# Kernel tuning notes

Hardware: AMD Instinct MI355X
Metric: run time of the kernel (lower is better)

Reference implementation:

```python
import jax, jax.numpy as jnp
import numpy as np

B, FIN, N, K, FOUT = 8, 64, 2048, 20, 128
BN_EPS = 1e-5
LEAKY_SLOPE = 0.01


def _conv2d(x, w, b):
    # x: [B,C,H,W], w: [O,I,kh,kw] -> valid conv, stride 1
    y = jax.lax.conv_general_dilated(
        x, w, window_strides=(1, 1), padding='VALID',
        dimension_numbers=('NCHW', 'OIHW', 'NCHW'))
    return y + b[None, :, None, None]


def _batchnorm(x, gamma, beta):
    # training-mode BN: batch stats over (B,H,W), biased variance (torch default)
    mean = jnp.mean(x, axis=(0, 2, 3), keepdims=True)
    var = jnp.var(x, axis=(0, 2, 3), keepdims=True)
    xn = (x - mean) * jax.lax.rsqrt(var + BN_EPS)
    return xn * gamma[None, :, None, None] + beta[None, :, None, None]


def _edge_features(x, k):
    # x: [B, D, N] -> [B, 2D, N, k]
    xt = jnp.transpose(x, (0, 2, 1))                      # [B,N,D]
    sq = jnp.sum(xt * xt, axis=-1)                        # [B,N]
    dist = sq[:, :, None] + sq[:, None, :] - 2.0 * jnp.einsum('bnd,bmd->bnm', xt, xt)
    # smallest k+1 distances (self is the smallest); drop self
    _, idx = jax.lax.top_k(-dist, k + 1)                  # [B,N,k+1]
    idx = idx[:, :, 1:]                                   # [B,N,k]
    nb = jax.vmap(lambda pts, ind: pts[ind])(xt, idx)     # [B,N,k,D]
    neighbors = jnp.transpose(nb, (0, 3, 1, 2))           # [B,D,N,k]
    central = x[:, :, :, None]                            # [B,D,N,1]
    central_k = jnp.broadcast_to(central, neighbors.shape)
    return jnp.concatenate([central_k, neighbors - central], axis=1)


def setup_inputs() -> dict:
    key = jax.random.key(0)
    ks = jax.random.split(key, 4)
    x = jax.random.normal(ks[0], (B, FIN, N), dtype=jnp.float32)
    conv1_w = jax.random.normal(ks[1], (4 * FIN, 2 * FIN, 1, K // 2 + 1), dtype=jnp.float32) * 0.02
    conv1_b = jnp.zeros((4 * FIN,), jnp.float32)
    bn1_g = jnp.ones((4 * FIN,), jnp.float32)
    bn1_b = jnp.zeros((4 * FIN,), jnp.float32)
    conv2_w = jax.random.normal(ks[2], (2 * FOUT, 2 * FIN, 1, 2 * K), dtype=jnp.float32) * 0.02
    conv2_b = jnp.zeros((2 * FOUT,), jnp.float32)
    bn2_g = jnp.ones((2 * FOUT,), jnp.float32)
    bn2_b = jnp.zeros((2 * FOUT,), jnp.float32)
    return {"x": x, "conv1_w": conv1_w, "conv1_b": conv1_b, "bn1_g": bn1_g,
            "bn1_b": bn1_b, "conv2_w": conv2_w, "conv2_b": conv2_b,
            "bn2_g": bn2_g, "bn2_b": bn2_b, "k": K}


def reference(x, conv1_w, conv1_b, bn1_g, bn1_b, conv2_w, conv2_b, bn2_g, bn2_b, k):
    ee = _edge_features(x, k)                             # [B,2Fin,N,k]
    Bb, CC, NN, KK = ee.shape
    # inte_conv_hk: conv [1, k//2+1] -> [B,4Fin,N,k/2], BN, LeakyReLU
    h = _batchnorm(_conv2d(ee, conv1_w, conv1_b), bn1_g, bn1_b)
    h = jnp.where(h > 0, h, LEAKY_SLOPE * h)
    # transpose/view dance: [B,N,4Fin,k/2] -> [B,N,2Fin,k] -> [B,2Fin,N,k]
    inte = jnp.transpose(h, (0, 2, 1, 3)).reshape(Bb, NN, CC, KK)
    inte = jnp.transpose(inte, (0, 2, 1, 3))
    merge = jnp.concatenate([ee, inte], axis=3)           # [B,2Fin,N,2k]
    y = _batchnorm(_conv2d(merge, conv2_w, conv2_b), bn2_g, bn2_b)
    y = jax.nn.relu(y)                                    # [B,2Fout,N,1]
    fout = y.shape[1] // 2
    return y.reshape(Bb, fout, 2 * NN)                    # [B,Fout,2N]
```

## Files before the change

kernel.cpp:

```cpp
#include <hip/hip_runtime.h>
#include <stdint.h>

typedef unsigned int uint;
typedef unsigned short ushort;
typedef __attribute__((ext_vector_type(8))) short short8;
typedef __attribute__((ext_vector_type(4))) float f32x4;

__device__ __forceinline__ uint f2bf(float f) {
  uint u = __float_as_uint(f);
  return (u + 0x7fffu + ((u >> 16) & 1u)) >> 16;
}
__device__ __forceinline__ float bf2f(uint us) {
  return __uint_as_float(us << 16);
}
__device__ __forceinline__ int lt_count(unsigned long long m) {
  return (int)__builtin_amdgcn_mbcnt_hi((uint)(m >> 32),
             __builtin_amdgcn_mbcnt_lo((uint)m, 0u));
}

__global__ __launch_bounds__(256) void prep_weights(
    const float* __restrict__ w1, const float* __restrict__ w2,
    ushort* __restrict__ wp1, ushort* __restrict__ wpack) {
  int g = blockIdx.x * 256 + threadIdx.x;
  if (g < 196608) {
    int chunk = g >> 9;
    int r = g & 511;
    int lane = r >> 3, j = r & 7;
    int tks = chunk >> 4;
    int ctile = chunk & 15;
    int t = tks >> 1, ks = tks & 1;
    int c = ctile * 16 + (lane & 15);
    int d = ks * 32 + ((lane >> 4) << 3) + j;
    float val;
    if (t < 11) {
      val = w1[c * 1408 + (64 + d) * 11 + t];
    } else {
      float s = 0.f;
      for (int tt = 0; tt < 11; ++tt)
        s += w1[c * 1408 + d * 11 + tt] - w1[c * 1408 + (64 + d) * 11 + tt];
      val = s;
    }
    wp1[g] = (ushort)f2bf(val);
  } else {
    int gp = g - 196608;
    int chunk = gp >> 9;
    int r = gp & 511;
    int lane = r >> 3, j = r & 7;
    int kb = chunk >> 5;
    int rem = chunk & 31;
    int ks = rem >> 4, ctile = rem & 15;
    int c = ctile * 16 + (lane & 15);
    int k = kb * 64 + ks * 32 + ((lane >> 4) << 3) + j;
    float val;
    if (k < 64) {
      int d = k;
      float s = 0.f;
      for (int jn = 0; jn < 20; ++jn)
        s += w2[c * 5120 + d * 40 + jn] - w2[c * 5120 + (64 + d) * 40 + jn];
      val = s;
    } else if (k < 1344) {
      int q = k - 64; int jn = q >> 6, d = q & 63;
      val = w2[c * 5120 + (64 + d) * 40 + jn];
    } else {
      int q = k - 1344; int ci = q / 20, jj = q - ci * 20;
      val = w2[c * 5120 + ci * 40 + 20 + jj];
    }
    wpack[gp] = (ushort)f2bf(val);
  }
}

__global__ __launch_bounds__(256) void transpose_x(const float* __restrict__ x,
                                                   uint* __restrict__ xtu,
                                                   float* __restrict__ xtf,
                                                   float* __restrict__ sqf) {
  __shared__ float t[64][65];
  int tid = threadIdx.x;
  int blk = blockIdx.x;
  int b = blk >> 5, n0 = (blk & 31) << 6;
  const float* xb = x + b * 131072;
  #pragma unroll
  for (int it = 0; it < 16; ++it) {
    int d = (it << 2) + (tid >> 6);
    int n = tid & 63;
    t[d][n] = xb[d * 2048 + n0 + n];
  }
  __syncthreads();
  #pragma unroll
  for (int it = 0; it < 8; ++it) {
    int n = (it << 3) + (tid >> 5);
    int dp = tid & 31;
    float f0 = t[2 * dp][n], f1 = t[2 * dp + 1][n];
    uint v = f2bf(f0) | (f2bf(f1) << 16);
    size_t col = (size_t)(b * 2048 + n0 + n);
    xtu[col * 32 + dp] = v;
    float2 fv; fv.x = f0; fv.y = f1;
    *(float2*)&xtf[(col << 6) + 2 * dp] = fv;
    float s = f0 * f0 + f1 * f1;
    #pragma unroll
    for (int off = 16; off > 0; off >>= 1) s += __shfl_xor(s, off);
    if (dp == 0) sqf[col] = s;
  }
}

__global__ __launch_bounds__(1024) void knn_kernel(
    const ushort* __restrict__ xbf_t, const float* __restrict__ sqf,
    int* __restrict__ cbuf) {
  __shared__ uint dist[16][1024];
  __shared__ uint surv[16][132];
  int tid = threadIdx.x;
  int wv = tid >> 6, lane = tid & 63;
  int grp = blockIdx.x >> 1;
  int half = blockIdx.x & 1;
  int cbase = half << 10;
  int row0 = grp << 4;
  int b = row0 >> 11, n0 = row0 & 2047;
  const ushort* xt = xbf_t + ((size_t)b << 17);
  const float* sqb = sqf + (b << 11);
  int m = lane & 15, quad = lane >> 4;
  short8 afr0 = *(const short8*)(xt + ((size_t)(n0 + m) << 6) + quad * 8);
  short8 afr1 = *(const short8*)(xt + ((size_t)(n0 + m) << 6) + 32 + quad * 8);
  for (int t = 0; t < 4; ++t) {
    int lcol = (((wv << 2) + t) << 4) + m;
    int col = cbase + lcol;
    short8 bfr0 = *(const short8*)(xt + ((size_t)col << 6) + quad * 8);
    short8 bfr1 = *(const short8*)(xt + ((size_t)col << 6) + 32 + quad * 8);
    f32x4 c = {};
    c = __builtin_amdgcn_mfma_f32_16x16x32_bf16(afr0, bfr0, c, 0, 0, 0);
    c = __builtin_amdgcn_mfma_f32_16x16x32_bf16(afr1, bfr1, c, 0, 0, 0);
    float sq = sqb[col];
    #pragma unroll
    for (int r = 0; r < 4; ++r) {
      float f = sq - 2.f * c[r];
      uint u = __float_as_uint(f);
      uint srt = u ^ ((uint)((int)u >> 31) | 0x80000000u);
      dist[quad * 4 + r][lcol] = (srt & 0xFFFFF800u) | (uint)col;
    }
  }
  __syncthreads();
  uint* dr = dist[wv];
  int selfl = (n0 + wv) - cbase;
  if (selfl >= 0 && selfl < 1024 && ((selfl & 63) == lane))
    dr[selfl] = 0xFFFFFFFFu;

  uint key[16];
  uint v0 = 0xFFFFFFFFu;
  #pragma unroll
  for (int l = 0; l < 16; ++l) {
    uint v = dr[(l << 6) + lane];
    key[l] = v;
    v0 = v0 < v ? v0 : v;
  }

  uint s = v0;
  #pragma unroll
  for (int k = 2; k <= 64; k <<= 1) {
    #pragma unroll
    for (int j = k >> 1; j > 0; j >>= 1) {
      uint o = (uint)__shfl_xor((int)s, j);
      bool up = ((lane & k) == 0);
      bool lower = ((lane & j) == 0);
      uint mn = s < o ? s : o;
      uint mx = s < o ? o : s;
      s = (lower == up) ? mn : mx;
    }
  }
  uint T = (uint)__shfl((int)s, 31);

  int base = 0;
  #pragma unroll
  for (int l = 0; l < 16; ++l) {
    uint v = key[l];
    bool f = (v <= T);
    unsigned long long mk = __ballot(f);
    if (f) {
      int pos = base + lt_count(mk);
      if (pos < 128) surv[wv][pos] = v;
    }
    base += __popcll(mk);
  }
  int S = base < 128 ? base : 128;
  if (lane < 4) surv[wv][S + lane] = 0xFFFFFFFFu;

  int outb = (row0 + wv) * 64 + (half << 5);
  uint k0 = (lane < S) ? surv[wv][lane] : 0xFFFFFFFFu;
  int r0 = 0;
  if (S > 64) {
    uint k1 = (lane + 64 < S) ? surv[wv][lane + 64] : 0xFFFFFFFFu;
    int r1 = 0;
    for (int i = 0; i < S; i += 4) {
      uint4 q = *(const uint4*)&surv[wv][i];
      r0 += (q.x < k0) + (q.y < k0) + (q.z < k0) + (q.w < k0);
      r1 += (q.x < k1) + (q.y < k1) + (q.z < k1) + (q.w < k1);
    }
    if (lane + 64 < S && r1 < 32) cbuf[outb + r1] = (int)(k1 & 2047u);
  } else {
    for (int i = 0; i < S; i += 4) {
      uint4 q = *(const uint4*)&surv[wv][i];
      r0 += (q.x < k0) + (q.y < k0) + (q.z < k0) + (q.w < k0);
    }
  }
  if (lane < S && r0 < 32) cbuf[outb + r0] = (int)(k0 & 2047u);
}

__global__ __launch_bounds__(256) void knn_merge(
    const float* __restrict__ xtf, const int* __restrict__ cbuf,
    int* __restrict__ idxout) {
  __shared__ double dkey[4][64];
  __shared__ int ccol[4][64];
  int tid = threadIdx.x;
  int wv = tid >> 6, lane = tid & 63;
  int row = (blockIdx.x << 2) + wv;
  int b = row >> 11, n = row & 2047;
  int ci = cbuf[row * 64 + lane];
  const float* xc = xtf + ((size_t)b << 17);
  const float4* xj4 = (const float4*)(xc + ((size_t)ci << 6));
  const float4* xi4 = (const float4*)(xc + ((size_t)n << 6));
  double dt = 0.0, s2 = 0.0;
  #pragma unroll 4
  for (int d4 = 0; d4 < 16; ++d4) {
    float4 vj = xj4[d4];
    float4 vi = xi4[d4];
    double a0 = (double)vj.x, a1 = (double)vj.y, a2 = (double)vj.z, a3 = (double)vj.w;
    s2 += a0 * a0 + a1 * a1 + a2 * a2 + a3 * a3;
    dt += (double)vi.x * a0 + (double)vi.y * a1 + (double)vi.z * a2 + (double)vi.w * a3;
  }
  dkey[wv][lane] = s2 - 2.0 * dt;
  ccol[wv][lane] = ci;
  __syncthreads();
  double kl = dkey[wv][lane];
  int rank = 0;
  for (int mm = 0; mm < 64; ++mm) {
    double km = dkey[wv][mm];
    int cm = ccol[wv][mm];
    if (km < kl || (km == kl && cm < ci)) ++rank;
  }
  if (rank < 20) idxout[row * 20 + rank] = ci;
}

__global__ __launch_bounds__(512, 4) void conv1_mfma(
    const ushort* __restrict__ xbf_t, const int* __restrict__ idxbuf,
    const ushort* __restrict__ wp1, uint* __restrict__ hu,
    float* __restrict__ stats) {
  __shared__ ushort sl[21][8][16][8];
  __shared__ int nidx[16][20];
  int tid = threadIdx.x;
  int p0 = blockIdx.x << 4;
  int b = p0 >> 11, n0 = p0 & 2047;
  const ushort* xt = xbf_t + ((size_t)b << 17);
  for (int v = tid; v < 320; v += 512) {
    int p = v / 20, j = v - p * 20;
    nidx[p][j] = idxbuf[(p0 + p) * 20 + j];
  }
  __syncthreads();
  for (int v = tid; v < 2688; v += 512) {
    int s = v >> 7;
    int r = v & 127;
    int p = r >> 3, i = r & 7;
    int col = (s == 0) ? (n0 + p) : nidx[p][s - 1];
    *(short8*)&sl[s][i][p ^ i][0] =
        *(const short8*)(xt + ((size_t)col << 6) + (i << 3));
  }
  __syncthreads();
  int lane = tid & 63, wave = tid >> 6;
  int m = lane & 15, quad = lane >> 4;
  #pragma unroll 1
  for (int pass = 0; pass < 2; ++pass) {
    int ctile = (pass << 3) + wave;
    int c = ctile * 16 + m;
    f32x4 acc[10] = {};
    f32x4 cacc = {};
    #pragma unroll 1
    for (int ks = 0; ks < 2; ++ks) {
      int cch = ks * 4 + quad;
      int ms = m ^ cch;
      short8 tb[11];
      #pragma unroll
      for (int t = 0; t < 11; ++t)
        tb[t] = *(const short8*)(wp1 + (((t * 2 + ks) * 16 + ctile) << 9) + lane * 8);
      short8 ub = *(const short8*)(wp1 + (((22 + ks) * 16 + ctile) << 9) + lane * 8);
      {
        short8 a = *(const short8*)&sl[0][cch][ms][0];
        cacc = __builtin_amdgcn_mfma_f32_16x16x32_bf16(a, ub, cacc, 0, 0, 0);
      }
      #pragma unroll
      for (int s = 1; s <= 20; ++s) {
        short8 a = *(const short8*)&sl[s][cch][ms][0];
        #pragma unroll
        for (int t = 0; t < 11; ++t) {
          int ko = s - 1 - t;
          if (ko >= 0 && ko < 10)
            acc[ko] = __builtin_amdgcn_mfma_f32_16x16x32_bf16(a, tb[t], acc[ko], 0, 0, 0);
        }
      }
    }
    float sacc = 0.f, ssacc = 0.f;
    #pragma unroll
    for (int r = 0; r < 4; ++r) {
      int p = (quad << 2) + r;
      int base5 = ((p0 + p) * 256 + c) * 5;
      float cc = cacc[r];
      #pragma unroll
      for (int q = 0; q < 5; ++q) {
        float f0 = acc[2 * q][r] + cc;
        float f1 = acc[2 * q + 1][r] + cc;
        sacc += f0 + f1;
        ssacc += f0 * f0 + f1 * f1;
        hu[base5 + q] = f2bf(f0) | (f2bf(f1) << 16);
      }
    }
    sacc += __shfl_xor(sacc, 16);  sacc += __shfl_xor(sacc, 32);
    ssacc += __shfl_xor(ssacc, 16); ssacc += __shfl_xor(ssacc, 32);
    if (quad == 0) {
      atomicAdd(&stats[c], sacc);
      atomicAdd(&stats[256 + c], ssacc);
    }
  }
}

__global__ void finalize_kernel(const float* __restrict__ stats,
                                const float* __restrict__ gamma,
                                const float* __restrict__ beta,
                                float* __restrict__ coef, float inv_count) {
  int c = threadIdx.x;
  float m = stats[c] * inv_count;
  float var = stats[256 + c] * inv_count - m * m;
  float a = gamma[c] * rsqrtf(var + 1e-5f);
  coef[c] = a;
  coef[256 + c] = beta[c] - m * a;
}

__global__ __launch_bounds__(512) void conv2_mfma(
    const ushort* __restrict__ xbf_t, const int* __restrict__ idxbuf,
    const uint* __restrict__ hu, const float* __restrict__ coef1,
    const ushort* __restrict__ wpack, float* __restrict__ yraw,
    float* __restrict__ stats) {
  __shared__ ushort As[2][4][64][72];
  __shared__ int nidx[64][20];
  __shared__ float cf[512];
  int tid = threadIdx.x;
  int p0 = blockIdx.x << 6;
  int b = p0 >> 11, n0 = p0 & 2047;
  const ushort* xt = xbf_t + ((size_t)b << 17);

  cf[tid] = coef1[tid];
  for (int v = tid; v < 1280; v += 512) {
    int p = v / 20, j = v - p * 20;
    nidx[p][j] = idxbuf[(p0 + p) * 20 + j];
  }
  __syncthreads();

  int pp = tid >> 3;
  int off = (tid & 7) << 3;

  auto build = [&](int phase, int buf) {
    int kb0 = phase << 2;
    short8 xv[4];
    uint4 hv[4];
    #pragma unroll
    for (int kc = 0; kc < 4; ++kc) {
      int kb = kb0 + kc;
      if (kb >= 61) continue;
      if (kb < 21) {
        int col = (kb == 0) ? (n0 + pp) : nidx[pp][kb - 1];
        xv[kc] = *(const short8*)(xt + ((size_t)col << 6) + off);
      } else {
        int q0 = (kb - 21) * 64 + off;
        hv[kc] = *(const uint4*)(hu + (size_t)(p0 + pp) * 1280 + (q0 >> 1));
      }
    }
    #pragma unroll
    for (int kc = 0; kc < 4; ++kc) {
      int kb = kb0 + kc;
      if (kb >= 61) continue;
      if (kb < 21) {
        *(short8*)&As[buf][kc][pp][off] = xv[kc];
      } else {
        int q0 = (kb - 21) * 64 + off;
        uint4 hvv = hv[kc];
        float f[8];
        f[0] = bf2f(hvv.x & 0xffffu); f[1] = bf2f(hvv.x >> 16);
        f[2] = bf2f(hvv.y & 0xffffu); f[3] = bf2f(hvv.y >> 16);
        f[4] = bf2f(hvv.z & 0xffffu); f[5] = bf2f(hvv.z >> 16);
        f[6] = bf2f(hvv.w & 0xffffu); f[7] = bf2f(hvv.w >> 16);
        ushort o[8];
        #pragma unroll
        for (int i = 0; i < 8; ++i) {
          int ch = (q0 + i) / 10;
          float vv = f[i] * cf[ch] + cf[256 + ch];
          vv = vv > 0.f ? vv : 0.01f * vv;
          o[i] = (ushort)f2bf(vv);
        }
        *(short8*)&As[buf][kc][pp][off] = *(short8*)o;
      }
    }
  };

  int lane = tid & 63, wave = tid >> 6;
  int m = lane & 15, quad = lane >> 4;
  f32x4 acc[4][2] = {};

  build(0, 0);
  __syncthreads();
  for (int phase = 0; phase < 16; ++phase) {
    int buf = phase & 1;
    if (phase < 15) build(phase + 1, buf ^ 1);
    #pragma unroll
    for (int kc = 0; kc < 4; ++kc) {
      int kb = (phase << 2) + kc;
      if (kb >= 61) break;
      #pragma unroll
      for (int ks = 0; ks < 2; ++ks) {
        short8 afr[4];
        #pragma unroll
        for (int mt = 0; mt < 4; ++mt)
          afr[mt] = *(const short8*)&As[buf][kc][mt * 16 + m][ks * 32 + quad * 8];
        #pragma unroll
        for (int nt = 0; nt < 2; ++nt) {
          const ushort* bp = wpack +
              (((size_t)((kb * 2 + ks) * 16 + (wave << 1) + nt)) << 9) + lane * 8;
          short8 bfr = *(const short8*)bp;
          #pragma unroll
          for (int mt = 0; mt < 4; ++mt)
            acc[mt][nt] = __builtin_amdgcn_mfma_f32_16x16x32_bf16(afr[mt], bfr, acc[mt][nt], 0, 0, 0);
        }
      }
    }
    __syncthreads();
  }
  #pragma unroll
  for (int nt = 0; nt < 2; ++nt) {
    int col = (wave << 5) + nt * 16 + m;
    float sacc = 0.f, ssacc = 0.f;
    #pragma unroll
    for (int mt = 0; mt < 4; ++mt) {
      #pragma unroll
      for (int r = 0; r < 4; ++r) {
        int prow = mt * 16 + quad * 4 + r;
        float v = acc[mt][nt][r];
        sacc += v; ssacc += v * v;
        yraw[(size_t)(p0 + prow) * 256 + col] = v;
      }
    }
    sacc += __shfl_xor(sacc, 16);  sacc += __shfl_xor(sacc, 32);
    ssacc += __shfl_xor(ssacc, 16); ssacc += __shfl_xor(ssacc, 32);
    if (quad == 0) {
      atomicAdd(&stats[col], sacc);
      atomicAdd(&stats[256 + col], ssacc);
    }
  }
}

__global__ __launch_bounds__(256) void out_kernel(const float* __restrict__ yraw,
                                                  const float* __restrict__ coef2,
                                                  float* __restrict__ out) {
  __shared__ float t[64][257];
  int tid = threadIdx.x;
  int blk = blockIdx.x;
  int b = blk >> 5, n0 = (blk & 31) << 6;
  for (int it = 0; it < 64; ++it)
    t[it][tid] = yraw[(b * 2048 + n0 + it) * 256 + tid];
  __syncthreads();
  int nsub = tid & 63, cq = tid >> 6;
  for (int it = 0; it < 64; ++it) {
    int c = (it << 2) + cq;
    float v = coef2[c] * t[nsub][c] + coef2[256 + c];
    out[(b * 256 + c) * 2048 + n0 + nsub] = v > 0.f ? v : 0.f;
  }
}

extern "C" void kernel_launch(void* const* d_in, const int* in_sizes, int n_in,
                              void* d_out, int out_size, void* d_ws, size_t ws_size,
                              hipStream_t stream) {
  const float* x   = (const float*)d_in[0];
  const float* w1  = (const float*)d_in[1];
  const float* g1  = (const float*)d_in[3];
  const float* be1 = (const float*)d_in[4];
  const float* w2  = (const float*)d_in[5];
  const float* g2  = (const float*)d_in[7];
  const float* be2 = (const float*)d_in[8];
  float* out = (float*)d_out;
  char* w = (char*)d_ws;
  float* sqf    = (float*)(w);
  int*  idxbuf  = (int*)(w + 131072);
  uint* hu      = (uint*)(w + 1441792);
  float* xtf    = (float*)(w + 1441792);
  int*  cbuf    = (int*)(w + 9830400);
  float* yraw   = (float*)(w + 85327872);
  float* stats  = (float*)(w + 102105088);
  float* coef   = (float*)(w + 102109184);
  ushort* wp1   = (ushort*)(w + 102113280);
  ushort* wpack = (ushort*)(w + 102506496);
  ushort* xbf_t = (ushort*)(w + 104505344);

  hipMemsetAsync(stats, 0, 4096, stream);
  prep_weights<<<4672, 256, 0, stream>>>(w1, w2, wp1, wpack);
  transpose_x<<<256, 256, 0, stream>>>(x, (uint*)xbf_t, xtf, sqf);
  knn_kernel<<<2048, 1024, 0, stream>>>(xbf_t, sqf, cbuf);
  knn_merge<<<4096, 256, 0, stream>>>(xtf, cbuf, idxbuf);
  conv1_mfma<<<1024, 512, 0, stream>>>(xbf_t, idxbuf, wp1, hu, stats);
  finalize_kernel<<<1, 256, 0, stream>>>(stats, g1, be1, coef, 1.f / 163840.f);
  conv2_mfma<<<256, 512, 0, stream>>>(xbf_t, idxbuf, hu, coef, wpack, yraw, stats + 512);
  finalize_kernel<<<1, 256, 0, stream>>>(stats + 512, g2, be2, coef + 512, 1.f / 16384.f);
  out_kernel<<<256, 256, 0, stream>>>(yraw, coef + 512, out);
}
```

Before: 325.1 us.

## Split conv2 output channels across two blocks, XOR-swizzle LDS, simplify BN channel lookup

conv2 now launches twice as many blocks, with each block computing half of the 256 output channels for 64 points. This halves the per-wave accumulators and raises occupancy (launch bounds 512,4) on a grid that previously had only 256 blocks. The A tile loses its padding and uses an XOR swizzle to avoid LDS bank conflicts. The per-element divide by 10 in the BN1 apply is replaced with a two-channel select. The cost is that the A-tile gather and BN1 apply are now done twice per point block.

```diff
diff --git a/kernel.cpp b/kernel.cpp
--- a/kernel.cpp
+++ b/kernel.cpp
@@ -329,20 +329,25 @@
   coef[256 + c] = beta[c] - m * a;
 }
 
-__global__ __launch_bounds__(512) void conv2_mfma(
+__global__ __launch_bounds__(512, 4) void conv2_mfma(
     const ushort* __restrict__ xbf_t, const int* __restrict__ idxbuf,
     const uint* __restrict__ hu, const float* __restrict__ coef1,
     const ushort* __restrict__ wpack, float* __restrict__ yraw,
     float* __restrict__ stats) {
-  __shared__ ushort As[2][4][64][72];
+  __shared__ ushort As[2][4][64][64];
   __shared__ int nidx[64][20];
-  __shared__ float cf[512];
+  __shared__ float cfA[257], cfB[257];
   int tid = threadIdx.x;
-  int p0 = blockIdx.x << 6;
+  int nblk = blockIdx.x & 1;
+  int p0 = (blockIdx.x >> 1) << 6;
   int b = p0 >> 11, n0 = p0 & 2047;
   const ushort* xt = xbf_t + ((size_t)b << 17);
 
-  cf[tid] = coef1[tid];
+  if (tid < 256) {
+    cfA[tid] = coef1[tid];
+    cfB[tid] = coef1[256 + tid];
+    if (tid == 0) { cfA[256] = 0.f; cfB[256] = 0.f; }
+  }
   for (int v = tid; v < 1280; v += 512) {
     int p = v / 20, j = v - p * 20;
     nidx[p][j] = idxbuf[(p0 + p) * 20 + j];
@@ -350,7 +355,9 @@
   __syncthreads();
 
   int pp = tid >> 3;
-  int off = (tid & 7) << 3;
+  int t7 = tid & 7;
+  int off = t7 << 3;
+  int wroff = ((t7 ^ (pp & 7)) << 3);
 
   auto build = [&](int phase, int buf) {
     int kb0 = phase << 2;
@@ -373,7 +380,7 @@
       int kb = kb0 + kc;
       if (kb >= 61) continue;
       if (kb < 21) {
-        *(short8*)&As[buf][kc][pp][off] = xv[kc];
+        *(short8*)&As[buf][kc][pp][wroff] = xv[kc];
       } else {
         int q0 = (kb - 21) * 64 + off;
         uint4 hvv = hv[kc];
@@ -382,22 +389,28 @@
         f[2] = bf2f(hvv.y & 0xffffu); f[3] = bf2f(hvv.y >> 16);
         f[4] = bf2f(hvv.z & 0xffffu); f[5] = bf2f(hvv.z >> 16);
         f[6] = bf2f(hvv.w & 0xffffu); f[7] = bf2f(hvv.w >> 16);
+        int ch0 = q0 / 10;
+        int rem = q0 - ch0 * 10;
+        float a0 = cfA[ch0], b0 = cfB[ch0];
+        float a1 = cfA[ch0 + 1], b1 = cfB[ch0 + 1];
         ushort o[8];
         #pragma unroll
         for (int i = 0; i < 8; ++i) {
-          int ch = (q0 + i) / 10;
-          float vv = f[i] * cf[ch] + cf[256 + ch];
+          bool hi = (rem + i) >= 10;
+          float vv = f[i] * (hi ? a1 : a0) + (hi ? b1 : b0);
           vv = vv > 0.f ? vv : 0.01f * vv;
           o[i] = (ushort)f2bf(vv);
         }
-        *(short8*)&As[buf][kc][pp][off] = *(short8*)o;
+        *(short8*)&As[buf][kc][pp][wroff] = *(short8*)o;
       }
     }
   };
 
   int lane = tid & 63, wave = tid >> 6;
   int m = lane & 15, quad = lane >> 4;
-  f32x4 acc[4][2] = {};
+  int rdoff0 = ((quad ^ (m & 7)) << 3);
+  int rdoff1 = (((4 + quad) ^ (m & 7)) << 3);
+  f32x4 acc[4] = {};
 
   build(0, 0);
   __syncthreads();
@@ -410,33 +423,30 @@
       if (kb >= 61) break;
       #pragma unroll
       for (int ks = 0; ks < 2; ++ks) {
+        int rdoff = ks ? rdoff1 : rdoff0;
         short8 afr[4];
         #pragma unroll
         for (int mt = 0; mt < 4; ++mt)
-          afr[mt] = *(const short8*)&As[buf][kc][mt * 16 + m][ks * 32 + quad * 8];
+          afr[mt] = *(const short8*)&As[buf][kc][mt * 16 + m][rdoff];
+        const ushort* bp = wpack +
+            (((size_t)((kb * 2 + ks) * 16 + (nblk << 3) + wave)) << 9) + lane * 8;
+        short8 bfr = *(const short8*)bp;
         #pragma unroll
-        for (int nt = 0; nt < 2; ++nt) {
-          const ushort* bp = wpack +
-              (((size_t)((kb * 2 + ks) * 16 + (wave << 1) + nt)) << 9) + lane * 8;
-          short8 bfr = *(const short8*)bp;
-          #pragma unroll
-          for (int mt = 0; mt < 4; ++mt)
-            acc[mt][nt] = __builtin_amdgcn_mfma_f32_16x16x32_bf16(afr[mt], bfr, acc[mt][nt], 0, 0, 0);
-        }
+        for (int mt = 0; mt < 4; ++mt)
+          acc[mt] = __builtin_amdgcn_mfma_f32_16x16x32_bf16(afr[mt], bfr, acc[mt], 0, 0, 0);
       }
     }
     __syncthreads();
   }
-  #pragma unroll
-  for (int nt = 0; nt < 2; ++nt) {
-    int col = (wave << 5) + nt * 16 + m;
+  {
+    int col = (nblk << 7) + (wave << 4) + m;
     float sacc = 0.f, ssacc = 0.f;
     #pragma unroll
     for (int mt = 0; mt < 4; ++mt) {
       #pragma unroll
       for (int r = 0; r < 4; ++r) {
         int prow = mt * 16 + quad * 4 + r;
-        float v = acc[mt][nt][r];
+        float v = acc[mt][r];
         sacc += v; ssacc += v * v;
         yraw[(size_t)(p0 + prow) * 256 + col] = v;
       }
@@ -499,7 +509,7 @@
   knn_merge<<<4096, 256, 0, stream>>>(xtf, cbuf, idxbuf);
   conv1_mfma<<<1024, 512, 0, stream>>>(xbf_t, idxbuf, wp1, hu, stats);
   finalize_kernel<<<1, 256, 0, stream>>>(stats, g1, be1, coef, 1.f / 163840.f);
-  conv2_mfma<<<256, 512, 0, stream>>>(xbf_t, idxbuf, hu, coef, wpack, yraw, stats + 512);
+  conv2_mfma<<<512, 512, 0, stream>>>(xbf_t, idxbuf, hu, coef, wpack, yraw, stats + 512);
   finalize_kernel<<<1, 256, 0, stream>>>(stats + 512, g2, be2, coef + 512, 1.f / 16384.f);
   out_kernel<<<256, 256, 0, stream>>>(yraw, coef + 512, out);
 }
```

After: 306.8 us. -5.6%, faster.
